# Optimization experiments

Measured on AMD Instinct MI355X. Metric: run time of the kernel, lower is better.

The kernel has to match this reference:

```python
import jax, jax.numpy as jnp
import numpy as np

EPS = 1e-15
N_NODES = 20000
N_EDGES = 640000
FEAT = 128
N_RBF = 20
CUTOFF = 5.0


def setup_inputs() -> dict:
    key = jax.random.key(0)
    ks = jax.random.split(key, 10)
    s_j = jax.random.normal(ks[0], (N_NODES, FEAT), jnp.float32)
    v_j = jax.random.normal(ks[1], (N_NODES, FEAT, 3), jnp.float32)
    r_ij = jax.random.normal(ks[2], (N_EDGES, 3), jnp.float32)
    nbrs = jax.random.randint(ks[3], (N_EDGES, 2), 0, N_NODES, jnp.int64)
    # InvariantDense: Dense(F->F, swish) then Dense(F->3F)
    W1 = jax.random.normal(ks[4], (FEAT, FEAT), jnp.float32) / np.sqrt(FEAT)
    b1 = jnp.zeros((FEAT,), jnp.float32)
    W2 = jax.random.normal(ks[5], (FEAT, 3 * FEAT), jnp.float32) / np.sqrt(FEAT)
    b2 = jnp.zeros((3 * FEAT,), jnp.float32)
    # DistanceEmbed dense: Dense(n_rbf -> 3F)
    Wd = jax.random.normal(ks[6], (N_RBF, 3 * FEAT), jnp.float32) / np.sqrt(N_RBF)
    bd = jnp.zeros((3 * FEAT,), jnp.float32)
    return {"s_j": s_j, "v_j": v_j, "r_ij": r_ij, "nbrs": nbrs,
            "W1": W1, "b1": b1, "W2": W2, "b2": b2, "Wd": Wd, "bd": bd}


def reference(s_j, v_j, r_ij, nbrs, W1, b1, W2, b2, Wd, bd):
    N, F = s_j.shape
    # preprocess_r
    dist = jnp.sqrt(jnp.sum(r_ij ** 2 + EPS, axis=-1))          # [E]
    unit = r_ij / dist[:, None]                                  # [E,3]
    # InvariantDense on nodes (dense before gather, as in torch code)
    phi_node = jax.nn.silu(s_j @ W1 + b1) @ W2 + b2              # [N,3F]
    phi = phi_node[nbrs[:, 1]]                                   # [E,3F]
    # PaiNN radial basis: sin(n*pi*d/cutoff)/d, n=1..n_rbf
    k = jnp.arange(1, N_RBF + 1, dtype=dist.dtype) * (np.pi / CUTOFF)  # [n_rbf]
    rbf = jnp.sin(dist[:, None] * k[None, :]) / dist[:, None]    # [E,n_rbf]
    # cosine cutoff envelope
    env = 0.5 * (jnp.cos(np.pi * dist / CUTOFF) + 1.0)
    env = jnp.where(dist < CUTOFF, env, 0.0)                     # [E]
    w_s = (rbf @ Wd + bd) * env[:, None]                         # [E,3F]
    inv = (phi * w_s).reshape(-1, 3, F)                          # [E,3,F]
    split0 = inv[:, 0, :][:, :, None]                            # [E,F,1]
    split1 = inv[:, 1, :]                                        # [E,F]
    split2 = inv[:, 2, :][:, :, None]                            # [E,F,1]
    delta_v_ij = split2 * unit[:, None, :] + split0 * v_j[nbrs[:, 1]]  # [E,F,3]
    idx = nbrs[:, 0]
    delta_s_i = jax.ops.segment_sum(split1, idx, num_segments=N)      # [N,F]
    delta_v_i = jax.ops.segment_sum(delta_v_ij, idx, num_segments=N)  # [N,F,3]
    return (delta_s_i, delta_v_i)
```

## Files before the change

### kernel.cpp

```cpp
#include <hip/hip_runtime.h>
#include <hip/hip_bf16.h>
#include <math.h>

typedef __hip_bfloat16 bf16;

#define FEAT 128
#define NRBF 20
#define CUTOFF_F 5.0f
#define KSCALE 0.62831853071795864769f
#define NB 4096
#define INV_H 819.0f
#define H_STEP 0.001221001221001221f

__device__ __forceinline__ float b2f(bf16 x) { return __bfloat162float(x); }
__device__ __forceinline__ bf16 f2b(float x) { return __float2bfloat16(x); }
__device__ __forceinline__ float us2f(unsigned short u) {
    return __uint_as_float(((unsigned)u) << 16);
}

template<int F32>
__device__ __forceinline__ float LD(const void* p, size_t i) {
    if (F32) return ((const float*)p)[i];
    return b2f(((const bf16*)p)[i]);
}
template<int F32>
__device__ __forceinline__ void ST(void* p, size_t i, float v) {
    if (F32) ((float*)p)[i] = v;
    else ((bf16*)p)[i] = f2b(v);
}

__device__ __forceinline__ int get_dst(const int* nb, int e, int is64) {
    return is64 ? nb[4 * e] : nb[2 * e];
}
__device__ __forceinline__ int get_src(const int* nb, int e, int is64) {
    return is64 ? nb[4 * e + 2] : nb[2 * e + 1];
}
__device__ __forceinline__ int clampi(int v, int n) {
    return v < 0 ? 0 : (v >= n ? n - 1 : v);
}

__global__ void init_kernel(const void* __restrict__ s_ptr, const int* __restrict__ nbrs32,
                            int nE, int* __restrict__ flags, int* __restrict__ counts, int nN) {
    int t = blockIdx.x * blockDim.x + threadIdx.x;
    if (t < nN) counts[t] = 0;
    if (t == 0) {
        const unsigned* u = (const unsigned*)s_ptr;
        int hits = 0;
        for (int i = 0; i < 64; ++i) {
            unsigned ef = (u[i] >> 7) & 0xFF;
            hits += (ef >= 110 && ef <= 135) ? 1 : 0;
        }
        flags[0] = (hits < 32) ? 1 : 0;
        int lim = 2 * nE; if (lim > 128) lim = 128;
        int allz = 1;
        for (int i = 1; i < lim; i += 2) allz &= (nbrs32[i] == 0);
        flags[1] = allz;
    }
}

__global__ void hist_kernel(const int* __restrict__ nbrs, const int* __restrict__ flags,
                            int* __restrict__ counts, int nE, int nN) {
    int e = blockIdx.x * blockDim.x + threadIdx.x;
    if (e < nE) {
        int d = clampi(get_dst(nbrs, e, flags[1]), nN);
        atomicAdd(&counts[d], 1);
    }
}

__global__ __launch_bounds__(1024) void scan_kernel(const int* __restrict__ counts,
        int* __restrict__ offsets, int* __restrict__ cursor, int nN) {
    __shared__ int part[1024];
    const int t = threadIdx.x;
    const int chunk = (nN + 1023) / 1024;
    const int base = t * chunk;
    int local[32];
    int sum = 0;
    for (int c = 0; c < chunk && c < 32; ++c) {
        int idx = base + c;
        int v = (idx < nN) ? counts[idx] : 0;
        local[c] = v;
        sum += v;
    }
    part[t] = sum;
    __syncthreads();
    for (int off = 1; off < 1024; off <<= 1) {
        int add = (t >= off) ? part[t - off] : 0;
        __syncthreads();
        part[t] += add;
        __syncthreads();
    }
    int run = part[t] - sum;
    for (int c = 0; c < chunk && c < 32; ++c) {
        int idx = base + c;
        if (idx < nN) { offsets[idx] = run; cursor[idx] = run; run += local[c]; }
    }
    if (t == 1023) offsets[nN] = part[1023];
}

__global__ __launch_bounds__(384) void prep_kernel(const void* __restrict__ Wd,
        const void* __restrict__ bd, float* __restrict__ WdT, const int* __restrict__ flags) {
    const int c = threadIdx.x;
    const int F32 = flags[0];
    if (F32) {
        for (int k = 0; k < NRBF; ++k) WdT[c * 24 + k] = ((const float*)Wd)[k * 384 + c];
        WdT[c * 24 + 20] = ((const float*)bd)[c];
    } else {
        for (int k = 0; k < NRBF; ++k) WdT[c * 24 + k] = b2f(((const bf16*)Wd)[k * 384 + c]);
        WdT[c * 24 + 20] = b2f(((const bf16*)bd)[c]);
    }
    WdT[c * 24 + 21] = 0.f; WdT[c * 24 + 22] = 0.f; WdT[c * 24 + 23] = 0.f;
}

__global__ __launch_bounds__(384) void build_table_kernel(const float* __restrict__ WdT,
        bf16* __restrict__ tab) {
    const int b = blockIdx.x;
    const int c = threadIdx.x;
    const float d = fmaxf(b * H_STEP, 1e-7f);
    const float x = d * KSCALE;
    const float s1 = sinf(x);
    const float c1 = cosf(x);
    const float env = (d < CUTOFF_F) ? (0.5f * (c1 + 1.0f)) : 0.0f;
    const float invd = 1.0f / d;
    float g[NRBF];
    const float tc = 2.0f * c1;
    float skm2 = 0.f, skm1 = s1;
    g[0] = s1 * invd;
    #pragma unroll
    for (int k = 1; k < NRBF; ++k) {
        const float sk = fmaf(tc, skm1, -skm2);
        g[k] = sk * invd;
        skm2 = skm1; skm1 = sk;
    }
    const float* w = WdT + (size_t)c * 24;
    float acc = w[20];
    #pragma unroll
    for (int k = 0; k < NRBF; ++k) acc = fmaf(g[k], w[k], acc);
    tab[(size_t)b * 384 + c] = f2b(acc * env);
}

template<int F32, int MODE>
__device__ void pre_scatter_body(const void* __restrict__ r_ij, const int* __restrict__ nbrs,
        int is64, int* __restrict__ cursor, int* __restrict__ src_ids,
        float4* __restrict__ u_env, int* __restrict__ pos_of_e, float* __restrict__ gbuf,
        int e, int nE, int nN) {
    const int d = clampi(get_dst(nbrs, e, is64), nN);
    const int j = clampi(get_src(nbrs, e, is64), nN);
    int pos = atomicAdd(&cursor[d], 1);
    pos = clampi(pos, nE);
    src_ids[pos] = j;

    const float rx = LD<F32>(r_ij, (size_t)3 * e + 0);
    const float ry = LD<F32>(r_ij, (size_t)3 * e + 1);
    const float rz = LD<F32>(r_ij, (size_t)3 * e + 2);
    const float d2   = rx * rx + ry * ry + rz * rz + 3e-15f;
    const float invd = rsqrtf(d2);
    const float dd   = d2 * invd;

    if (MODE == 2) {
        u_env[pos] = make_float4(rx * invd, ry * invd, rz * invd, dd);
        return;
    }

    const float x  = dd * KSCALE;
    const float c1 = F32 ? cosf(x) : __cosf(x);
    const float env = (dd < CUTOFF_F) ? (0.5f * (c1 + 1.0f)) : 0.0f;
    u_env[pos] = make_float4(rx * invd, ry * invd, rz * invd, env);

    if (MODE == 1) {
        pos_of_e[e] = pos;
    } else {
        const float s1 = F32 ? sinf(x) : __sinf(x);
        const float scale = invd * env;
        const float tc = 2.0f * c1;
        float skm2 = 0.f, skm1 = s1;
        float* g = gbuf + (size_t)pos * NRBF;
        g[0] = s1 * scale;
        #pragma unroll
        for (int k = 1; k < NRBF; ++k) {
            const float sk = fmaf(tc, skm1, -skm2);
            g[k] = sk * scale;
            skm2 = skm1; skm1 = sk;
        }
    }
}

__global__ __launch_bounds__(256) void pre_scatter_kernel(const void* r_ij, const int* nbrs,
        const int* __restrict__ flags, int* cursor, int* src_ids, float4* u_env,
        int* pos_of_e, float* gbuf, int nE, int nN, int mode) {
    int e = blockIdx.x * blockDim.x + threadIdx.x;
    if (e >= nE) return;
    const int F32 = flags[0], is64 = flags[1];
    if (mode == 2) {
        if (F32) pre_scatter_body<1,2>(r_ij, nbrs, is64, cursor, src_ids, u_env, pos_of_e, gbuf, e, nE, nN);
        else     pre_scatter_body<0,2>(r_ij, nbrs, is64, cursor, src_ids, u_env, pos_of_e, gbuf, e, nE, nN);
    } else if (mode == 1) {
        if (F32) pre_scatter_body<1,1>(r_ij, nbrs, is64, cursor, src_ids, u_env, pos_of_e, gbuf, e, nE, nN);
        else     pre_scatter_body<0,1>(r_ij, nbrs, is64, cursor, src_ids, u_env, pos_of_e, gbuf, e, nE, nN);
    } else {
        if (F32) pre_scatter_body<1,0>(r_ij, nbrs, is64, cursor, src_ids, u_env, pos_of_e, gbuf, e, nE, nN);
        else     pre_scatter_body<0,0>(r_ij, nbrs, is64, cursor, src_ids, u_env, pos_of_e, gbuf, e, nE, nN);
    }
}

template<int F32>
__device__ void gemm_body(const void* __restrict__ s_j, const void* __restrict__ W1,
                          const void* __restrict__ b1, const void* __restrict__ W2,
                          const void* __restrict__ b2v, bf16* __restrict__ phi, int nN,
                          int packed) {
    __shared__ float sl[8][FEAT];
    __shared__ float hl[8][FEAT];
    const int t = threadIdx.x;
    const int n0 = blockIdx.x * 8;
    for (int idx = t; idx < 8 * FEAT; idx += 384) {
        int n = idx >> 7, k = idx & 127;
        int row = n0 + n;
        sl[n][k] = (row < nN) ? LD<F32>(s_j, (size_t)row * FEAT + k) : 0.f;
    }
    __syncthreads();
    for (int idx = t; idx < 8 * FEAT; idx += 384) {
        int n = idx >> 7, f = idx & 127;
        float a = 0.f;
        #pragma unroll 4
        for (int k = 0; k < FEAT; ++k) a = fmaf(sl[n][k], LD<F32>(W1, (size_t)k * FEAT + f), a);
        a += LD<F32>(b1, f);
        float sg = F32 ? (1.0f / (1.0f + expf(-a))) : (1.0f / (1.0f + __expf(-a)));
        hl[n][f] = a * sg;
    }
    __syncthreads();
    float acc[8] = {};
    #pragma unroll 4
    for (int k = 0; k < FEAT; ++k) {
        const float w = LD<F32>(W2, (size_t)k * 384 + t);
        #pragma unroll
        for (int n = 0; n < 8; ++n) acc[n] = fmaf(hl[n][k], w, acc[n]);
    }
    const float bb = LD<F32>(b2v, t);
    const int fch  = t & 127;
    const int comp = t >> 7;
    #pragma unroll
    for (int n = 0; n < 8; ++n) {
        int row = n0 + n;
        if (row < nN) {
            if (packed) phi[((size_t)row * FEAT + fch) * 8 + comp] = f2b(acc[n] + bb);
            else        phi[(size_t)row * 384 + t] = f2b(acc[n] + bb);
        }
    }
}

__global__ __launch_bounds__(384) void gemm_node_kernel(const void* s_j, const void* W1,
        const void* b1, const void* W2, const void* b2v, bf16* phi,
        const int* __restrict__ flags, int nN, int packed) {
    if (flags[0]) gemm_body<1>(s_j, W1, b1, W2, b2v, phi, nN, packed);
    else          gemm_body<0>(s_j, W1, b1, W2, b2v, phi, nN, packed);
}

__global__ __launch_bounds__(256) void pack_v_kernel(const void* __restrict__ v_j,
        bf16* __restrict__ rec, const int* __restrict__ flags, int nN) {
    int t = blockIdx.x * blockDim.x + threadIdx.x;
    if (t >= nN * FEAT) return;
    float vx, vy, vz;
    if (flags[0]) {
        const float* v = (const float*)v_j;
        vx = v[(size_t)3 * t + 0];
        vy = v[(size_t)3 * t + 1];
        vz = v[(size_t)3 * t + 2];
    } else {
        const bf16* v = (const bf16*)v_j;
        vx = b2f(v[(size_t)3 * t + 0]);
        vy = b2f(v[(size_t)3 * t + 1]);
        vz = b2f(v[(size_t)3 * t + 2]);
    }
    bf16* d = rec + (size_t)t * 8;
    union { bf16 b[2]; unsigned u; } p01;
    p01.b[0] = f2b(vx); p01.b[1] = f2b(vy);
    *(unsigned*)(d + 4) = p01.u;
    d[6] = f2b(vz);
}

template<int F32>
__device__ void pre_ws_body(const void* __restrict__ r_ij, const float* __restrict__ WdT,
        const int* __restrict__ pos_of_e, bf16* __restrict__ ws_w, int e) {
    const float rx = LD<F32>(r_ij, (size_t)3 * e + 0);
    const float ry = LD<F32>(r_ij, (size_t)3 * e + 1);
    const float rz = LD<F32>(r_ij, (size_t)3 * e + 2);
    const float d2   = rx * rx + ry * ry + rz * rz + 3e-15f;
    const float invd = rsqrtf(d2);
    const float dd   = d2 * invd;
    const float x  = dd * KSCALE;
    const float s1 = F32 ? sinf(x) : __sinf(x);
    const float c1 = F32 ? cosf(x) : __cosf(x);
    const float env = (dd < CUTOFF_F) ? (0.5f * (c1 + 1.0f)) : 0.0f;
    const float scale = invd * env;
    float gk[NRBF];
    const float tc = 2.0f * c1;
    float skm2 = 0.f, skm1 = s1;
    gk[0] = s1 * scale;
    #pragma unroll
    for (int k = 1; k < NRBF; ++k) {
        const float sk = fmaf(tc, skm1, -skm2);
        gk[k] = sk * scale;
        skm2 = skm1; skm1 = sk;
    }
    const int pos = pos_of_e[e];
    bf16* dst = ws_w + (size_t)pos * 384;
    for (int c0 = 0; c0 < 384; c0 += 4) {
        float r[4];
        #pragma unroll
        for (int u = 0; u < 4; ++u) {
            const float* w = WdT + (size_t)(c0 + u) * 24;
            float acc = w[20] * env;
            #pragma unroll
            for (int k = 0; k < NRBF; ++k) acc = fmaf(gk[k], w[k], acc);
            r[u] = acc;
        }
        union { bf16 b[4]; uint2 u2; } pk;
        pk.b[0] = f2b(r[0]); pk.b[1] = f2b(r[1]); pk.b[2] = f2b(r[2]); pk.b[3] = f2b(r[3]);
        *(uint2*)(dst + c0) = pk.u2;
    }
}

__global__ __launch_bounds__(256) void pre_ws_kernel(const void* r_ij,
        const float* __restrict__ WdT, const int* __restrict__ pos_of_e,
        bf16* __restrict__ ws_w, const int* __restrict__ flags, int nE) {
    int e = blockIdx.x * blockDim.x + threadIdx.x;
    if (e >= nE) return;
    if (flags[0]) pre_ws_body<1>(r_ij, WdT, pos_of_e, ws_w, e);
    else          pre_ws_body<0>(r_ij, WdT, pos_of_e, ws_w, e);
}

template<int F32>
__device__ void msg_a_body(const bf16* __restrict__ ws_w, const bf16* __restrict__ phi,
        const void* __restrict__ v_j, const int* __restrict__ src_ids,
        const float4* __restrict__ u_env, const int* __restrict__ offsets,
        void* __restrict__ out, int nE, int nN) {
    const int i = blockIdx.x;
    const int f = threadIdx.x;
    int start = offsets[i];
    int end   = offsets[i + 1];
    if (start < 0) start = 0;
    if (end > nE) end = nE;

    float ds = 0.f, dv0 = 0.f, dv1 = 0.f, dv2 = 0.f;

    #pragma unroll 2
    for (int p = start; p < end; ++p) {
        const int j = src_ids[p];
        const float4 ue = u_env[p];
        const bf16* wr = ws_w + (size_t)p * 384;
        const float w0 = b2f(wr[f]);
        const float w1 = b2f(wr[FEAT + f]);
        const float w2 = b2f(wr[2 * FEAT + f]);
        const bf16* ph = phi + (size_t)j * 384;
        const float p0 = b2f(ph[f]);
        const float p1 = b2f(ph[FEAT + f]);
        const float p2 = b2f(ph[2 * FEAT + f]);
        const float vx = LD<F32>(v_j, ((size_t)j * FEAT + f) * 3 + 0);
        const float vy = LD<F32>(v_j, ((size_t)j * FEAT + f) * 3 + 1);
        const float vz = LD<F32>(v_j, ((size_t)j * FEAT + f) * 3 + 2);
        const float i0 = w0 * p0;
        const float i1 = w1 * p1;
        const float i2 = w2 * p2;
        ds += i1;
        dv0 = fmaf(i2, ue.x, fmaf(i0, vx, dv0));
        dv1 = fmaf(i2, ue.y, fmaf(i0, vy, dv1));
        dv2 = fmaf(i2, ue.z, fmaf(i0, vz, dv2));
    }

    ST<F32>(out, (size_t)i * FEAT + f, ds);
    const size_t ob = (size_t)nN * FEAT + ((size_t)i * FEAT + f) * 3;
    ST<F32>(out, ob + 0, dv0);
    ST<F32>(out, ob + 1, dv1);
    ST<F32>(out, ob + 2, dv2);
}

__global__ __launch_bounds__(128) void msg_a_kernel(const bf16* ws_w, const bf16* phi,
        const void* v_j, const int* src_ids, const float4* u_env, const int* offsets,
        const int* __restrict__ flags, void* out, int nE, int nN) {
    if (flags[0]) msg_a_body<1>(ws_w, phi, v_j, src_ids, u_env, offsets, out, nE, nN);
    else          msg_a_body<0>(ws_w, phi, v_j, src_ids, u_env, offsets, out, nE, nN);
}

template<int F32>
__device__ void msg_c_body(const unsigned short* __restrict__ tab, const bf16* __restrict__ rec,
        const int* __restrict__ src_ids, const float4* __restrict__ u_env,
        const int* __restrict__ offsets, void* __restrict__ out, int nE, int nN) {
    const int i = blockIdx.x;
    const int f = threadIdx.x;
    int start = offsets[i];
    int end   = offsets[i + 1];
    if (start < 0) start = 0;
    if (end > nE) end = nE;

    float ds = 0.f, dv0 = 0.f, dv1 = 0.f, dv2 = 0.f;

    for (int p = start; p < end; ++p) {
        const int j = src_ids[p];
        const float4 ue = u_env[p];
        const float d = ue.w;
        const float binf = d * INV_H;
        int bin = (int)binf;
        if (bin > NB - 2) bin = NB - 2;
        const float fr = binf - (float)bin;
        const float m = (d < CUTOFF_F) ? 1.0f : 0.0f;

        const unsigned short* T = tab + (size_t)bin * 384;
        const float t00 = us2f(T[f]);
        const float t01 = us2f(T[384 + f]);
        const float t10 = us2f(T[FEAT + f]);
        const float t11 = us2f(T[384 + FEAT + f]);
        const float t20 = us2f(T[2 * FEAT + f]);
        const float t21 = us2f(T[384 + 2 * FEAT + f]);
        const float w0 = fmaf(t01 - t00, fr, t00) * m;
        const float w1 = fmaf(t11 - t10, fr, t10) * m;
        const float w2 = fmaf(t21 - t20, fr, t20) * m;

        const uint4 rv = *(const uint4*)(rec + ((size_t)j * FEAT + f) * 8);
        const float p0 = __uint_as_float(rv.x << 16);
        const float p1 = __uint_as_float(rv.x & 0xffff0000u);
        const float p2 = __uint_as_float(rv.y << 16);
        const float vx = __uint_as_float(rv.z << 16);
        const float vy = __uint_as_float(rv.z & 0xffff0000u);
        const float vz = __uint_as_float(rv.w << 16);

        const float i0 = w0 * p0;
        const float i1 = w1 * p1;
        const float i2 = w2 * p2;
        ds += i1;
        dv0 = fmaf(i2, ue.x, fmaf(i0, vx, dv0));
        dv1 = fmaf(i2, ue.y, fmaf(i0, vy, dv1));
        dv2 = fmaf(i2, ue.z, fmaf(i0, vz, dv2));
    }

    ST<F32>(out, (size_t)i * FEAT + f, ds);
    const size_t ob = (size_t)nN * FEAT + ((size_t)i * FEAT + f) * 3;
    ST<F32>(out, ob + 0, dv0);
    ST<F32>(out, ob + 1, dv1);
    ST<F32>(out, ob + 2, dv2);
}

__global__ __launch_bounds__(128) void msg_c_kernel(const unsigned short* tab, const bf16* rec,
        const int* src_ids, const float4* u_env, const int* offsets,
        const int* __restrict__ flags, void* out, int nE, int nN) {
    if (flags[0]) msg_c_body<1>(tab, rec, src_ids, u_env, offsets, out, nE, nN);
    else          msg_c_body<0>(tab, rec, src_ids, u_env, offsets, out, nE, nN);
}

template<int F32>
__device__ void msg_b_body(const void* __restrict__ v_j, const void* __restrict__ Wd,
        const void* __restrict__ bd, const bf16* __restrict__ phi,
        const float* __restrict__ gbuf, const int* __restrict__ src_ids,
        const float4* __restrict__ u_env, const int* __restrict__ offsets,
        void* __restrict__ out, int nE, int nN) {
    const int i = blockIdx.x;
    const int f = threadIdx.x;

    float wd0[NRBF], wd1[NRBF], wd2[NRBF];
    #pragma unroll
    for (int k = 0; k < NRBF; ++k) {
        wd0[k] = LD<F32>(Wd, (size_t)k * 384 + f);
        wd1[k] = LD<F32>(Wd, (size_t)k * 384 + FEAT + f);
        wd2[k] = LD<F32>(Wd, (size_t)k * 384 + 2 * FEAT + f);
    }
    const float bd0 = LD<F32>(bd, f);
    const float bd1 = LD<F32>(bd, FEAT + f);
    const float bd2 = LD<F32>(bd, 2 * FEAT + f);

    int start = offsets[i];
    int end   = offsets[i + 1];
    if (start < 0) start = 0;
    if (end > nE) end = nE;

    float ds = 0.f, dv0 = 0.f, dv1 = 0.f, dv2 = 0.f;

    for (int p = start; p < end; ++p) {
        const int j = src_ids[p];
        const float4 ue = u_env[p];
        const float* g = gbuf + (size_t)p * NRBF;
        float t0 = 0.f, t1 = 0.f, t2 = 0.f;
        #pragma unroll
        for (int k = 0; k < NRBF; ++k) {
            const float gk = g[k];
            t0 = fmaf(gk, wd0[k], t0);
            t1 = fmaf(gk, wd1[k], t1);
            t2 = fmaf(gk, wd2[k], t2);
        }
        const float w0 = fmaf(bd0, ue.w, t0);
        const float w1 = fmaf(bd1, ue.w, t1);
        const float w2 = fmaf(bd2, ue.w, t2);

        const bf16* ph = phi + (size_t)j * 384;
        const float p0 = b2f(ph[f]);
        const float p1 = b2f(ph[FEAT + f]);
        const float p2 = b2f(ph[2 * FEAT + f]);
        const float vx = LD<F32>(v_j, ((size_t)j * FEAT + f) * 3 + 0);
        const float vy = LD<F32>(v_j, ((size_t)j * FEAT + f) * 3 + 1);
        const float vz = LD<F32>(v_j, ((size_t)j * FEAT + f) * 3 + 2);

        const float i0 = w0 * p0;
        const float i1 = w1 * p1;
        const float i2 = w2 * p2;
        ds += i1;
        dv0 = fmaf(i2, ue.x, fmaf(i0, vx, dv0));
        dv1 = fmaf(i2, ue.y, fmaf(i0, vy, dv1));
        dv2 = fmaf(i2, ue.z, fmaf(i0, vz, dv2));
    }

    ST<F32>(out, (size_t)i * FEAT + f, ds);
    const size_t ob = (size_t)nN * FEAT + ((size_t)i * FEAT + f) * 3;
    ST<F32>(out, ob + 0, dv0);
    ST<F32>(out, ob + 1, dv1);
    ST<F32>(out, ob + 2, dv2);
}

__global__ __launch_bounds__(128) void msg_b_kernel(const void* v_j, const void* Wd,
        const void* bd, const bf16* phi, const float* gbuf, const int* src_ids,
        const float4* u_env, const int* offsets, const int* __restrict__ flags,
        void* out, int nE, int nN) {
    if (flags[0]) msg_b_body<1>(v_j, Wd, bd, phi, gbuf, src_ids, u_env, offsets, out, nE, nN);
    else          msg_b_body<0>(v_j, Wd, bd, phi, gbuf, src_ids, u_env, offsets, out, nE, nN);
}

extern "C" void kernel_launch(void* const* d_in, const int* in_sizes, int n_in,
                              void* d_out, int out_size, void* d_ws, size_t ws_size,
                              hipStream_t stream) {
    const void* s_j  = d_in[0];
    const void* v_j  = d_in[1];
    const void* r_ij = d_in[2];
    const int*  nbrs = (const int*)d_in[3];
    const void* W1   = d_in[4];
    const void* b1   = d_in[5];
    const void* W2   = d_in[6];
    const void* b2   = d_in[7];
    const void* Wd   = d_in[8];
    const void* bd   = d_in[9];

    const int nN = out_size / (4 * FEAT);
    const int nE = in_sizes[2] / 3;

    char* ws = (char*)d_ws;
    size_t off = 0;
    auto alloc = [&](size_t bytes) -> void* {
        void* p = ws + off;
        off = (off + bytes + 255) & ~(size_t)255;
        return p;
    };
    int*    flags    = (int*)alloc(16);
    int*    counts   = (int*)alloc((size_t)nN * 4);
    int*    offsets  = (int*)alloc(((size_t)nN + 1) * 4);
    int*    cursor   = (int*)alloc((size_t)nN * 4);
    int*    src_ids  = (int*)alloc((size_t)nE * 4);
    float4* u_env    = (float4*)alloc((size_t)nE * 16);
    float*  WdT      = (float*)alloc((size_t)384 * 24 * 4);
    const size_t base = off;

    size_t offA = base;
    int*  pos_of_e = (int*)(ws + offA);  offA += ((size_t)nE * 4 + 255) & ~(size_t)255;
    bf16* phiA     = (bf16*)(ws + offA); offA += ((size_t)nN * 384 * 2 + 255) & ~(size_t)255;
    bf16* ws_w     = (bf16*)(ws + offA); offA += (size_t)nE * 384 * 2;
    size_t offC = base;
    bf16* rec = (bf16*)(ws + offC);      offC += ((size_t)nN * FEAT * 8 * 2 + 255) & ~(size_t)255;
    bf16* tab = (bf16*)(ws + offC);      offC += (size_t)NB * 384 * 2;
    size_t offB = base;
    float* gbufB = (float*)(ws + offB);  offB += ((size_t)nE * NRBF * 4 + 255) & ~(size_t)255;
    bf16*  phiB  = (bf16*)(ws + offB);   offB += (size_t)nN * 384 * 2;

    const int modeA = (ws_size >= offA) ? 1 : 0;
    const int modeC = (!modeA && ws_size >= offC) ? 1 : 0;

    init_kernel<<<(nN + 255) / 256, 256, 0, stream>>>(s_j, nbrs, nE, flags, counts, nN);
    hist_kernel<<<(nE + 255) / 256, 256, 0, stream>>>(nbrs, flags, counts, nE, nN);
    scan_kernel<<<1, 1024, 0, stream>>>(counts, offsets, cursor, nN);
    prep_kernel<<<1, 384, 0, stream>>>(Wd, bd, WdT, flags);

    const int psMode = modeA ? 1 : (modeC ? 2 : 0);
    pre_scatter_kernel<<<(nE + 255) / 256, 256, 0, stream>>>(
        r_ij, nbrs, flags, cursor, src_ids, u_env, pos_of_e, gbufB, nE, nN, psMode);

    if (modeA) {
        gemm_node_kernel<<<(nN + 7) / 8, 384, 0, stream>>>(s_j, W1, b1, W2, b2, phiA, flags, nN, 0);
        pre_ws_kernel<<<(nE + 255) / 256, 256, 0, stream>>>(r_ij, WdT, pos_of_e, ws_w, flags, nE);
        msg_a_kernel<<<nN, 128, 0, stream>>>(ws_w, phiA, v_j, src_ids, u_env, offsets,
                                             flags, d_out, nE, nN);
    } else if (modeC) {
        build_table_kernel<<<NB, 384, 0, stream>>>(WdT, tab);
        gemm_node_kernel<<<(nN + 7) / 8, 384, 0, stream>>>(s_j, W1, b1, W2, b2, rec, flags, nN, 1);
        pack_v_kernel<<<((nN * FEAT) + 255) / 256, 256, 0, stream>>>(v_j, rec, flags, nN);
        msg_c_kernel<<<nN, 128, 0, stream>>>((const unsigned short*)tab, rec, src_ids, u_env,
                                             offsets, flags, d_out, nE, nN);
    } else {
        gemm_node_kernel<<<(nN + 7) / 8, 384, 0, stream>>>(s_j, W1, b1, W2, b2, phiB, flags, nN, 0);
        msg_b_kernel<<<nN, 128, 0, stream>>>(v_j, Wd, bd, phiB, gbufB, src_ids, u_env,
                                             offsets, flags, d_out, nE, nN);
    }
}
```

Before: 538.7 us.

## Pack phi and v records into 6 bf16, fuse v packing, recompute geometry in message kernel

Shrinks each per-node feature record from 8 to 6 bf16 values and writes the v components inside the node GEMM kernel, which removes the separate pack_v kernel. The pre-scatter pass in mode C now stores only the original edge index per sorted position instead of a 16-byte unit/distance float4. The message kernel re-reads r_ij through that index and recomputes the unit vector and distance. This cuts gather bytes and one launch, at the cost of an extra indirect, uncoalesced r_ij read per edge and unaligned 4-byte loads in place of one uint4 load.

```diff
diff --git a/kernel.cpp b/kernel.cpp
--- a/kernel.cpp
+++ b/kernel.cpp
@@ -142,12 +142,17 @@
 __device__ void pre_scatter_body(const void* __restrict__ r_ij, const int* __restrict__ nbrs,
         int is64, int* __restrict__ cursor, int* __restrict__ src_ids,
         float4* __restrict__ u_env, int* __restrict__ pos_of_e, float* __restrict__ gbuf,
-        int e, int nE, int nN) {
+        int* __restrict__ epos, int e, int nE, int nN) {
     const int d = clampi(get_dst(nbrs, e, is64), nN);
     const int j = clampi(get_src(nbrs, e, is64), nN);
     int pos = atomicAdd(&cursor[d], 1);
     pos = clampi(pos, nE);
     src_ids[pos] = j;
+
+    if (MODE == 2) {
+        epos[pos] = e;
+        return;
+    }
 
     const float rx = LD<F32>(r_ij, (size_t)3 * e + 0);
     const float ry = LD<F32>(r_ij, (size_t)3 * e + 1);
@@ -155,12 +160,6 @@
     const float d2   = rx * rx + ry * ry + rz * rz + 3e-15f;
     const float invd = rsqrtf(d2);
     const float dd   = d2 * invd;
-
-    if (MODE == 2) {
-        u_env[pos] = make_float4(rx * invd, ry * invd, rz * invd, dd);
-        return;
-    }
-
     const float x  = dd * KSCALE;
     const float c1 = F32 ? cosf(x) : __cosf(x);
     const float env = (dd < CUTOFF_F) ? (0.5f * (c1 + 1.0f)) : 0.0f;
@@ -186,24 +185,25 @@
 
 __global__ __launch_bounds__(256) void pre_scatter_kernel(const void* r_ij, const int* nbrs,
         const int* __restrict__ flags, int* cursor, int* src_ids, float4* u_env,
-        int* pos_of_e, float* gbuf, int nE, int nN, int mode) {
+        int* pos_of_e, float* gbuf, int* epos, int nE, int nN, int mode) {
     int e = blockIdx.x * blockDim.x + threadIdx.x;
     if (e >= nE) return;
     const int F32 = flags[0], is64 = flags[1];
     if (mode == 2) {
-        if (F32) pre_scatter_body<1,2>(r_ij, nbrs, is64, cursor, src_ids, u_env, pos_of_e, gbuf, e, nE, nN);
-        else     pre_scatter_body<0,2>(r_ij, nbrs, is64, cursor, src_ids, u_env, pos_of_e, gbuf, e, nE, nN);
+        if (F32) pre_scatter_body<1,2>(r_ij, nbrs, is64, cursor, src_ids, u_env, pos_of_e, gbuf, epos, e, nE, nN);
+        else     pre_scatter_body<0,2>(r_ij, nbrs, is64, cursor, src_ids, u_env, pos_of_e, gbuf, epos, e, nE, nN);
     } else if (mode == 1) {
-        if (F32) pre_scatter_body<1,1>(r_ij, nbrs, is64, cursor, src_ids, u_env, pos_of_e, gbuf, e, nE, nN);
-        else     pre_scatter_body<0,1>(r_ij, nbrs, is64, cursor, src_ids, u_env, pos_of_e, gbuf, e, nE, nN);
+        if (F32) pre_scatter_body<1,1>(r_ij, nbrs, is64, cursor, src_ids, u_env, pos_of_e, gbuf, epos, e, nE, nN);
+        else     pre_scatter_body<0,1>(r_ij, nbrs, is64, cursor, src_ids, u_env, pos_of_e, gbuf, epos, e, nE, nN);
     } else {
-        if (F32) pre_scatter_body<1,0>(r_ij, nbrs, is64, cursor, src_ids, u_env, pos_of_e, gbuf, e, nE, nN);
-        else     pre_scatter_body<0,0>(r_ij, nbrs, is64, cursor, src_ids, u_env, pos_of_e, gbuf, e, nE, nN);
-    }
-}
-
-template<int F32>
-__device__ void gemm_body(const void* __restrict__ s_j, const void* __restrict__ W1,
+        if (F32) pre_scatter_body<1,0>(r_ij, nbrs, is64, cursor, src_ids, u_env, pos_of_e, gbuf, epos, e, nE, nN);
+        else     pre_scatter_body<0,0>(r_ij, nbrs, is64, cursor, src_ids, u_env, pos_of_e, gbuf, epos, e, nE, nN);
+    }
+}
+
+template<int F32>
+__device__ void gemm_body(const void* __restrict__ s_j, const void* __restrict__ v_j,
+                          const void* __restrict__ W1,
                           const void* __restrict__ b1, const void* __restrict__ W2,
                           const void* __restrict__ b2v, bf16* __restrict__ phi, int nN,
                           int packed) {
@@ -211,6 +211,20 @@
     __shared__ float hl[8][FEAT];
     const int t = threadIdx.x;
     const int n0 = blockIdx.x * 8;
+    const int fch  = t & 127;
+    const int comp = t >> 7;
+
+    if (packed) {
+        #pragma unroll
+        for (int n = 0; n < 8; ++n) {
+            int row = n0 + n;
+            if (row < nN) {
+                const float vv = LD<F32>(v_j, ((size_t)row * FEAT + fch) * 3 + comp);
+                phi[((size_t)row * FEAT + fch) * 6 + 3 + comp] = f2b(vv);
+            }
+        }
+    }
+
     for (int idx = t; idx < 8 * FEAT; idx += 384) {
         int n = idx >> 7, k = idx & 127;
         int row = n0 + n;
@@ -235,46 +249,21 @@
         for (int n = 0; n < 8; ++n) acc[n] = fmaf(hl[n][k], w, acc[n]);
     }
     const float bb = LD<F32>(b2v, t);
-    const int fch  = t & 127;
-    const int comp = t >> 7;
     #pragma unroll
     for (int n = 0; n < 8; ++n) {
         int row = n0 + n;
         if (row < nN) {
-            if (packed) phi[((size_t)row * FEAT + fch) * 8 + comp] = f2b(acc[n] + bb);
+            if (packed) phi[((size_t)row * FEAT + fch) * 6 + comp] = f2b(acc[n] + bb);
             else        phi[(size_t)row * 384 + t] = f2b(acc[n] + bb);
         }
     }
 }
 
-__global__ __launch_bounds__(384) void gemm_node_kernel(const void* s_j, const void* W1,
-        const void* b1, const void* W2, const void* b2v, bf16* phi,
+__global__ __launch_bounds__(384) void gemm_node_kernel(const void* s_j, const void* v_j,
+        const void* W1, const void* b1, const void* W2, const void* b2v, bf16* phi,
         const int* __restrict__ flags, int nN, int packed) {
-    if (flags[0]) gemm_body<1>(s_j, W1, b1, W2, b2v, phi, nN, packed);
-    else          gemm_body<0>(s_j, W1, b1, W2, b2v, phi, nN, packed);
-}
-
-__global__ __launch_bounds__(256) void pack_v_kernel(const void* __restrict__ v_j,
-        bf16* __restrict__ rec, const int* __restrict__ flags, int nN) {
-    int t = blockIdx.x * blockDim.x + threadIdx.x;
-    if (t >= nN * FEAT) return;
-    float vx, vy, vz;
-    if (flags[0]) {
-        const float* v = (const float*)v_j;
-        vx = v[(size_t)3 * t + 0];
-        vy = v[(size_t)3 * t + 1];
-        vz = v[(size_t)3 * t + 2];
-    } else {
-        const bf16* v = (const bf16*)v_j;
-        vx = b2f(v[(size_t)3 * t + 0]);
-        vy = b2f(v[(size_t)3 * t + 1]);
-        vz = b2f(v[(size_t)3 * t + 2]);
-    }
-    bf16* d = rec + (size_t)t * 8;
-    union { bf16 b[2]; unsigned u; } p01;
-    p01.b[0] = f2b(vx); p01.b[1] = f2b(vy);
-    *(unsigned*)(d + 4) = p01.u;
-    d[6] = f2b(vz);
+    if (flags[0]) gemm_body<1>(s_j, v_j, W1, b1, W2, b2v, phi, nN, packed);
+    else          gemm_body<0>(s_j, v_j, W1, b1, W2, b2v, phi, nN, packed);
 }
 
 template<int F32>
@@ -382,8 +371,9 @@
 
 template<int F32>
 __device__ void msg_c_body(const unsigned short* __restrict__ tab, const bf16* __restrict__ rec,
-        const int* __restrict__ src_ids, const float4* __restrict__ u_env,
-        const int* __restrict__ offsets, void* __restrict__ out, int nE, int nN) {
+        const void* __restrict__ r_ij, const int* __restrict__ src_ids,
+        const int* __restrict__ epos, const int* __restrict__ offsets,
+        void* __restrict__ out, int nE, int nN) {
     const int i = blockIdx.x;
     const int f = threadIdx.x;
     int start = offsets[i];
@@ -395,13 +385,20 @@
 
     for (int p = start; p < end; ++p) {
         const int j = src_ids[p];
-        const float4 ue = u_env[p];
-        const float d = ue.w;
-        const float binf = d * INV_H;
+        const int e = clampi(epos[p], nE);
+        const float rx = LD<F32>(r_ij, (size_t)3 * e + 0);
+        const float ry = LD<F32>(r_ij, (size_t)3 * e + 1);
+        const float rz = LD<F32>(r_ij, (size_t)3 * e + 2);
+        const float d2   = rx * rx + ry * ry + rz * rz + 3e-15f;
+        const float invd = rsqrtf(d2);
+        const float dd   = d2 * invd;
+        const float ux = rx * invd, uy = ry * invd, uz = rz * invd;
+
+        const float binf = dd * INV_H;
         int bin = (int)binf;
         if (bin > NB - 2) bin = NB - 2;
         const float fr = binf - (float)bin;
-        const float m = (d < CUTOFF_F) ? 1.0f : 0.0f;
+        const float m = (dd < CUTOFF_F) ? 1.0f : 0.0f;
 
         const unsigned short* T = tab + (size_t)bin * 384;
         const float t00 = us2f(T[f]);
@@ -414,21 +411,24 @@
         const float w1 = fmaf(t11 - t10, fr, t10) * m;
         const float w2 = fmaf(t21 - t20, fr, t20) * m;
 
-        const uint4 rv = *(const uint4*)(rec + ((size_t)j * FEAT + f) * 8);
-        const float p0 = __uint_as_float(rv.x << 16);
-        const float p1 = __uint_as_float(rv.x & 0xffff0000u);
-        const float p2 = __uint_as_float(rv.y << 16);
-        const float vx = __uint_as_float(rv.z << 16);
-        const float vy = __uint_as_float(rv.z & 0xffff0000u);
-        const float vz = __uint_as_float(rv.w << 16);
+        const unsigned* rp = (const unsigned*)(rec + ((size_t)j * FEAT + f) * 6);
+        const unsigned ra = rp[0];
+        const unsigned rb = rp[1];
+        const unsigned rc = rp[2];
+        const float p0 = __uint_as_float(ra << 16);
+        const float p1 = __uint_as_float(ra & 0xffff0000u);
+        const float p2 = __uint_as_float(rb << 16);
+        const float vx = __uint_as_float(rb & 0xffff0000u);
+        const float vy = __uint_as_float(rc << 16);
+        const float vz = __uint_as_float(rc & 0xffff0000u);
 
         const float i0 = w0 * p0;
         const float i1 = w1 * p1;
         const float i2 = w2 * p2;
         ds += i1;
-        dv0 = fmaf(i2, ue.x, fmaf(i0, vx, dv0));
-        dv1 = fmaf(i2, ue.y, fmaf(i0, vy, dv1));
-        dv2 = fmaf(i2, ue.z, fmaf(i0, vz, dv2));
+        dv0 = fmaf(i2, ux, fmaf(i0, vx, dv0));
+        dv1 = fmaf(i2, uy, fmaf(i0, vy, dv1));
+        dv2 = fmaf(i2, uz, fmaf(i0, vz, dv2));
     }
 
     ST<F32>(out, (size_t)i * FEAT + f, ds);
@@ -439,10 +439,10 @@
 }
 
 __global__ __launch_bounds__(128) void msg_c_kernel(const unsigned short* tab, const bf16* rec,
-        const int* src_ids, const float4* u_env, const int* offsets,
+        const void* r_ij, const int* src_ids, const int* epos, const int* offsets,
         const int* __restrict__ flags, void* out, int nE, int nN) {
-    if (flags[0]) msg_c_body<1>(tab, rec, src_ids, u_env, offsets, out, nE, nN);
-    else          msg_c_body<0>(tab, rec, src_ids, u_env, offsets, out, nE, nN);
+    if (flags[0]) msg_c_body<1>(tab, rec, r_ij, src_ids, epos, offsets, out, nE, nN);
+    else          msg_c_body<0>(tab, rec, r_ij, src_ids, epos, offsets, out, nE, nN);
 }
 
 template<int F32>
@@ -550,6 +550,7 @@
     int*    cursor   = (int*)alloc((size_t)nN * 4);
     int*    src_ids  = (int*)alloc((size_t)nE * 4);
     float4* u_env    = (float4*)alloc((size_t)nE * 16);
+    int*    epos     = (int*)alloc((size_t)nE * 4);
     float*  WdT      = (float*)alloc((size_t)384 * 24 * 4);
     const size_t base = off;
 
@@ -558,7 +559,7 @@
     bf16* phiA     = (bf16*)(ws + offA); offA += ((size_t)nN * 384 * 2 + 255) & ~(size_t)255;
     bf16* ws_w     = (bf16*)(ws + offA); offA += (size_t)nE * 384 * 2;
     size_t offC = base;
-    bf16* rec = (bf16*)(ws + offC);      offC += ((size_t)nN * FEAT * 8 * 2 + 255) & ~(size_t)255;
+    bf16* rec = (bf16*)(ws + offC);      offC += ((size_t)nN * FEAT * 6 * 2 + 255) & ~(size_t)255;
     bf16* tab = (bf16*)(ws + offC);      offC += (size_t)NB * 384 * 2;
     size_t offB = base;
     float* gbufB = (float*)(ws + offB);  offB += ((size_t)nE * NRBF * 4 + 255) & ~(size_t)255;
@@ -574,21 +575,20 @@
 
     const int psMode = modeA ? 1 : (modeC ? 2 : 0);
     pre_scatter_kernel<<<(nE + 255) / 256, 256, 0, stream>>>(
-        r_ij, nbrs, flags, cursor, src_ids, u_env, pos_of_e, gbufB, nE, nN, psMode);
+        r_ij, nbrs, flags, cursor, src_ids, u_env, pos_of_e, gbufB, epos, nE, nN, psMode);
 
     if (modeA) {
-        gemm_node_kernel<<<(nN + 7) / 8, 384, 0, stream>>>(s_j, W1, b1, W2, b2, phiA, flags, nN, 0);
+        gemm_node_kernel<<<(nN + 7) / 8, 384, 0, stream>>>(s_j, v_j, W1, b1, W2, b2, phiA, flags, nN, 0);
         pre_ws_kernel<<<(nE + 255) / 256, 256, 0, stream>>>(r_ij, WdT, pos_of_e, ws_w, flags, nE);
         msg_a_kernel<<<nN, 128, 0, stream>>>(ws_w, phiA, v_j, src_ids, u_env, offsets,
                                              flags, d_out, nE, nN);
     } else if (modeC) {
         build_table_kernel<<<NB, 384, 0, stream>>>(WdT, tab);
-        gemm_node_kernel<<<(nN + 7) / 8, 384, 0, stream>>>(s_j, W1, b1, W2, b2, rec, flags, nN, 1);
-        pack_v_kernel<<<((nN * FEAT) + 255) / 256, 256, 0, stream>>>(v_j, rec, flags, nN);
-        msg_c_kernel<<<nN, 128, 0, stream>>>((const unsigned short*)tab, rec, src_ids, u_env,
-                                             offsets, flags, d_out, nE, nN);
+        gemm_node_kernel<<<(nN + 7) / 8, 384, 0, stream>>>(s_j, v_j, W1, b1, W2, b2, rec, flags, nN, 1);
+        msg_c_kernel<<<nN, 128, 0, stream>>>((const unsigned short*)tab, rec, r_ij, src_ids,
+                                             epos, offsets, flags, d_out, nE, nN);
     } else {
-        gemm_node_kernel<<<(nN + 7) / 8, 384, 0, stream>>>(s_j, W1, b1, W2, b2, phiB, flags, nN, 0);
+        gemm_node_kernel<<<(nN + 7) / 8, 384, 0, stream>>>(s_j, v_j, W1, b1, W2, b2, phiB, flags, nN, 0);
         msg_b_kernel<<<nN, 128, 0, stream>>>(v_j, Wd, bd, phiB, gbufB, src_ids, u_env,
                                              offsets, flags, d_out, nE, nN);
     }
```

Measured after the change: 504.0 us. 6.4% less time.
